# Optimization experiments

Measured on AMD Instinct MI355X. Metric: run time of the kernel, lower is better.

The kernel has to match this reference:

```python
import jax, jax.numpy as jnp
import numpy as np

B, S, I, H, O = 64, 512, 256, 1024, 256


def setup_inputs() -> dict:
    key = jax.random.key(0)
    ks = jax.random.split(key, 12)
    s_in = 1.0 / np.sqrt(H)  # torch RNN init scale
    inp = {
        "x": jax.random.normal(ks[0], (B, S, I), dtype=jnp.float32),
        "W_ih_0": jax.random.uniform(ks[1], (H, I), jnp.float32, -s_in, s_in),
        "W_hh_0": jax.random.uniform(ks[2], (H, H), jnp.float32, -s_in, s_in),
        "b_ih_0": jax.random.uniform(ks[3], (H,), jnp.float32, -s_in, s_in),
        "b_hh_0": jax.random.uniform(ks[4], (H,), jnp.float32, -s_in, s_in),
        "W_ih_1": jax.random.uniform(ks[5], (H, H), jnp.float32, -s_in, s_in),
        "W_hh_1": jax.random.uniform(ks[6], (H, H), jnp.float32, -s_in, s_in),
        "b_ih_1": jax.random.uniform(ks[7], (H,), jnp.float32, -s_in, s_in),
        "b_hh_1": jax.random.uniform(ks[8], (H,), jnp.float32, -s_in, s_in),
        "fc_w": jax.random.uniform(ks[9], (O, H), jnp.float32, -s_in, s_in),
        "fc_b": jax.random.uniform(ks[10], (O,), jnp.float32, -s_in, s_in),
    }
    return inp


def _rnn_layer(inp, W_ih, W_hh, b_ih, b_hh):
    # Pre-compute input projection for all timesteps (one big GEMM),
    # then scan the sequential recurrence: h_t = tanh(Wx_t + U h_{t-1} + b)
    pre = jnp.einsum('bsi,hi->bsh', inp, W_ih) + (b_ih + b_hh)  # [B,S,H]
    h0 = jnp.zeros((inp.shape[0], W_hh.shape[0]), dtype=inp.dtype)

    def step(h, p_t):
        h = jnp.tanh(p_t + h @ W_hh.T)
        return h, h

    _, hs = jax.lax.scan(step, h0, jnp.swapaxes(pre, 0, 1))  # [S,B,H]
    return jnp.swapaxes(hs, 0, 1)  # [B,S,H]


def reference(x, W_ih_0, W_hh_0, b_ih_0, b_hh_0,
              W_ih_1, W_hh_1, b_ih_1, b_hh_1, fc_w, fc_b):
    h = _rnn_layer(x, W_ih_0, W_hh_0, b_ih_0, b_hh_0)
    h = _rnn_layer(h, W_ih_1, W_hh_1, b_ih_1, b_hh_1)
    return h @ fc_w.T + fc_b  # [B,S,O]
```

## Files before the change

### kernel.cpp

```cpp
#include <hip/hip_runtime.h>
#include <hip/hip_bf16.h>


typedef __attribute__((ext_vector_type(4))) float f32x4;
typedef __attribute__((ext_vector_type(8))) short bf16x8;
typedef __attribute__((ext_vector_type(4))) int   i32x4;
typedef __attribute__((ext_vector_type(4))) short s16x4;

#define B_  64
#define S_  512
#define I_  256
#define H_  1024
#define O_  256
#define M_  (B_ * S_)
#define SH_ (S_ * H_)

static __device__ __forceinline__ unsigned short f2bf(float f) {
  union { float f; unsigned u; } v; v.f = f;
  unsigned r = v.u + 0x7fffu + ((v.u >> 16) & 1u);
  return (unsigned short)(r >> 16);
}
static __device__ __forceinline__ float bf2f(unsigned short b) {
  union { unsigned u; float f; } v; v.u = ((unsigned)b) << 16;
  return v.f;
}
static __device__ __forceinline__ float tanh_fast(float x) {
  float e = __expf(2.f * x);
  return 1.f - 2.f / (e + 1.f);
}
static __device__ __forceinline__ bf16x8 as_bf16x8(i32x4 v) {
  union { i32x4 i; bf16x8 b; } u; u.i = v; return u.b;
}

__global__ void cvt_bf16(const float* __restrict__ src,
                         unsigned short* __restrict__ dst, int n4) {
  int i = blockIdx.x * blockDim.x + threadIdx.x;
  if (i < n4) {
    f32x4 v = ((const f32x4*)src)[i];
    s16x4 o;
    o[0] = (short)f2bf(v[0]); o[1] = (short)f2bf(v[1]);
    o[2] = (short)f2bf(v[2]); o[3] = (short)f2bf(v[3]);
    ((s16x4*)dst)[i] = o;
  }
}

template <bool BF16OUT>
__global__ __launch_bounds__(256)
void gemm_bf16(const unsigned short* __restrict__ A,
               const unsigned short* __restrict__ W,
               const float* __restrict__ b1, const float* __restrict__ b2,
               void* __restrict__ Cv, int Mx, int Nx, int Kx) {
  __shared__ __align__(16) unsigned short As[128 * 40];
  __shared__ __align__(16) unsigned short Bs[128 * 40];
  const int tid  = threadIdx.x;
  const int m0   = blockIdx.y * 128;
  const int n0   = blockIdx.x * 128;
  const int w    = tid >> 6, lane = tid & 63;
  const int quad = lane >> 4, l15 = lane & 15;
  const int wm = (w & 1) * 64, wn = (w >> 1) * 64;

  f32x4 acc[4][4] = {};

  for (int k0 = 0; k0 < Kx; k0 += 32) {
#pragma unroll
    for (int i = 0; i < 2; ++i) {
      int c = tid + i * 256;
      int row = c >> 2, kc = c & 3;
      *(i32x4*)&As[row * 40 + kc * 8] =
          *(const i32x4*)&A[(size_t)(m0 + row) * Kx + k0 + kc * 8];
      *(i32x4*)&Bs[row * 40 + kc * 8] =
          *(const i32x4*)&W[(size_t)(n0 + row) * Kx + k0 + kc * 8];
    }
    __syncthreads();
    bf16x8 af[4], bg[4];
#pragma unroll
    for (int im = 0; im < 4; ++im)
      af[im] = *(const bf16x8*)&As[(wm + im * 16 + l15) * 40 + quad * 8];
#pragma unroll
    for (int in = 0; in < 4; ++in)
      bg[in] = *(const bf16x8*)&Bs[(wn + in * 16 + l15) * 40 + quad * 8];
#pragma unroll
    for (int im = 0; im < 4; ++im)
#pragma unroll
      for (int in = 0; in < 4; ++in)
        acc[im][in] = __builtin_amdgcn_mfma_f32_16x16x32_bf16(
            af[im], bg[in], acc[im][in], 0, 0, 0);
    __syncthreads();
  }

#pragma unroll
  for (int in = 0; in < 4; ++in) {
    int n = n0 + wn + in * 16 + l15;
    float bv = b1 ? b1[n] : 0.f;
    if (b2) bv += b2[n];
#pragma unroll
    for (int im = 0; im < 4; ++im) {
      int mb = m0 + wm + im * 16 + quad * 4;
#pragma unroll
      for (int r = 0; r < 4; ++r) {
        float val = acc[im][in][r] + bv;
        size_t o = (size_t)(mb + r) * Nx + n;
        if (BF16OUT) ((unsigned short*)Cv)[o] = f2bf(val);
        else         ((float*)Cv)[o] = val;
      }
    }
  }
}

__global__ __launch_bounds__(256, 1)
void rnn_fused(const unsigned short* __restrict__ Whh0,
               const unsigned short* __restrict__ Wih1,
               const unsigned short* __restrict__ Whh1,
               const unsigned short* __restrict__ pre0,
               const float* __restrict__ b_ih_1,
               const float* __restrict__ b_hh_1,
               unsigned short* __restrict__ h0seq,
               unsigned short* __restrict__ h1seq,
               unsigned int* __restrict__ flags)
{
  const int bx   = blockIdx.x;
  const int tid  = threadIdx.x;
  const int w    = tid >> 6;
  const int lane = tid & 63;
  const int quad = lane >> 4, l15 = lane & 15;

  __shared__ __align__(16) float q[4][4][16][20];

  if (bx < 64) {
    const int g  = bx >> 4;
    const int n0 = (bx & 15) * 64;
    unsigned int* const f0 = flags + g * S_;

    i32x4 Wf[4][8];
    {
      const unsigned short* wp = Whh0 + (size_t)(n0 + l15) * H_ + w * 256 + quad * 8;
#pragma unroll
      for (int i = 0; i < 4; ++i)
#pragma unroll
        for (int kk = 0; kk < 8; ++kk)
          Wf[i][kk] = *(const i32x4*)(wp + (size_t)i * 16 * H_ + kk * 32);
    }
#pragma unroll
    for (int i = 0; i < 4; ++i)
#pragma unroll
      for (int kk = 0; kk < 8; ++kk)
        asm volatile("" : "+v"(Wf[i][kk]));

    for (int t = 0; t < S_; ++t) {
      float pv[4];
      {
        const unsigned short* pp = pre0 + (size_t)(g * 16 + quad * 4) * SH_ +
                                   (size_t)t * H_ + n0 + w * 16 + l15;
#pragma unroll
        for (int r = 0; r < 4; ++r) pv[r] = bf2f(pp[(size_t)r * SH_]);
      }

      f32x4 acc[4] = {};
      if (t > 0) {
        if (tid == 0) {
          while (__hip_atomic_load(&f0[t - 1], __ATOMIC_RELAXED,
                                   __HIP_MEMORY_SCOPE_AGENT) < 16u) {}
          __builtin_amdgcn_fence(__ATOMIC_ACQUIRE, "agent");
        }
        __syncthreads();
        const unsigned short* hp = h0seq + (size_t)(g * 16 + l15) * SH_ +
                                   (size_t)(t - 1) * H_ + w * 256 + quad * 8;
        bf16x8 Af[8];
#pragma unroll
        for (int kk = 0; kk < 8; ++kk) Af[kk] = *(const bf16x8*)(hp + kk * 32);
#pragma unroll
        for (int kk = 0; kk < 8; ++kk)
#pragma unroll
          for (int i = 0; i < 4; ++i)
            acc[i] = __builtin_amdgcn_mfma_f32_16x16x32_bf16(
                Af[kk], as_bf16x8(Wf[i][kk]), acc[i], 0, 0, 0);
      }

#pragma unroll
      for (int i = 0; i < 4; ++i) *(f32x4*)&q[w][i][l15][quad * 4] = acc[i];
      __syncthreads();
      f32x4 s = {};
#pragma unroll
      for (int wp2 = 0; wp2 < 4; ++wp2) {
        f32x4 v = *(const f32x4*)&q[wp2][w][l15][quad * 4];
#pragma unroll
        for (int r = 0; r < 4; ++r) s[r] += v[r];
      }

#pragma unroll
      for (int r = 0; r < 4; ++r) {
        unsigned short hb = f2bf(tanh_fast(pv[r] + s[r]));
        size_t o = (size_t)(g * 16 + quad * 4 + r) * SH_ + (size_t)t * H_ +
                   n0 + w * 16 + l15;
        __hip_atomic_store(&h0seq[o], hb, __ATOMIC_RELAXED,
                           __HIP_MEMORY_SCOPE_AGENT);
      }
      __syncthreads();
      if (tid == 0)
        __hip_atomic_fetch_add(&f0[t], 1u, __ATOMIC_RELAXED,
                               __HIP_MEMORY_SCOPE_AGENT);
    }
  } else {
    const int id = bx - 64;
    const int g  = id >> 5;
    const int n0 = (id & 31) * 32;
    unsigned int* const f0 = flags + g * S_;
    unsigned int* const f1 = flags + 4 * S_ + g * S_;

    i32x4 Wi[2][8], Wr[2][8];
    {
      const unsigned short* wpi = Wih1 + (size_t)(n0 + l15) * H_ + w * 256 + quad * 8;
      const unsigned short* wpr = Whh1 + (size_t)(n0 + l15) * H_ + w * 256 + quad * 8;
#pragma unroll
      for (int i = 0; i < 2; ++i)
#pragma unroll
        for (int kk = 0; kk < 8; ++kk) {
          Wi[i][kk] = *(const i32x4*)(wpi + (size_t)i * 16 * H_ + kk * 32);
          Wr[i][kk] = *(const i32x4*)(wpr + (size_t)i * 16 * H_ + kk * 32);
        }
    }
#pragma unroll
    for (int i = 0; i < 2; ++i)
#pragma unroll
      for (int kk = 0; kk < 8; ++kk) {
        asm volatile("" : "+v"(Wi[i][kk]));
        asm volatile("" : "+v"(Wr[i][kk]));
      }

    float bias = 0.f;
    if (w < 2) {
      int n = n0 + w * 16 + l15;
      bias = b_ih_1[n] + b_hh_1[n];
    }

    for (int t = 0; t < S_; ++t) {
      f32x4 acc[2] = {};

      if (tid == 0) {
        while (__hip_atomic_load(&f0[t], __ATOMIC_RELAXED,
                                 __HIP_MEMORY_SCOPE_AGENT) < 16u) {}
        __builtin_amdgcn_fence(__ATOMIC_ACQUIRE, "agent");
      }
      __syncthreads();
      {
        const unsigned short* hp = h0seq + (size_t)(g * 16 + l15) * SH_ +
                                   (size_t)t * H_ + w * 256 + quad * 8;
        bf16x8 Af[8];
#pragma unroll
        for (int kk = 0; kk < 8; ++kk) Af[kk] = *(const bf16x8*)(hp + kk * 32);
#pragma unroll
        for (int kk = 0; kk < 8; ++kk)
#pragma unroll
          for (int i = 0; i < 2; ++i)
            acc[i] = __builtin_amdgcn_mfma_f32_16x16x32_bf16(
                Af[kk], as_bf16x8(Wi[i][kk]), acc[i], 0, 0, 0);
      }

      if (t > 0) {
        if (tid == 0) {
          while (__hip_atomic_load(&f1[t - 1], __ATOMIC_RELAXED,
                                   __HIP_MEMORY_SCOPE_AGENT) < 32u) {}
          __builtin_amdgcn_fence(__ATOMIC_ACQUIRE, "agent");
        }
        __syncthreads();
        const unsigned short* hp = h1seq + (size_t)(g * 16 + l15) * SH_ +
                                   (size_t)(t - 1) * H_ + w * 256 + quad * 8;
        bf16x8 Af[8];
#pragma unroll
        for (int kk = 0; kk < 8; ++kk) Af[kk] = *(const bf16x8*)(hp + kk * 32);
#pragma unroll
        for (int kk = 0; kk < 8; ++kk)
#pragma unroll
          for (int i = 0; i < 2; ++i)
            acc[i] = __builtin_amdgcn_mfma_f32_16x16x32_bf16(
                Af[kk], as_bf16x8(Wr[i][kk]), acc[i], 0, 0, 0);
      }

#pragma unroll
      for (int i = 0; i < 2; ++i) *(f32x4*)&q[w][i][l15][quad * 4] = acc[i];
      __syncthreads();
      if (w < 2) {
        f32x4 s = {};
#pragma unroll
        for (int wp2 = 0; wp2 < 4; ++wp2) {
          f32x4 v = *(const f32x4*)&q[wp2][w][l15][quad * 4];
#pragma unroll
          for (int r = 0; r < 4; ++r) s[r] += v[r];
        }
#pragma unroll
        for (int r = 0; r < 4; ++r) {
          unsigned short hb = f2bf(tanh_fast(bias + s[r]));
          size_t o = (size_t)(g * 16 + quad * 4 + r) * SH_ + (size_t)t * H_ +
                     n0 + w * 16 + l15;
          __hip_atomic_store(&h1seq[o], hb, __ATOMIC_RELAXED,
                             __HIP_MEMORY_SCOPE_AGENT);
        }
      }
      __syncthreads();
      if (tid == 0)
        __hip_atomic_fetch_add(&f1[t], 1u, __ATOMIC_RELAXED,
                               __HIP_MEMORY_SCOPE_AGENT);
    }
  }
}

extern "C" void kernel_launch(void* const* d_in, const int* in_sizes, int n_in,
                              void* d_out, int out_size, void* d_ws, size_t ws_size,
                              hipStream_t stream) {
  const float* x      = (const float*)d_in[0];
  const float* W_ih_0 = (const float*)d_in[1];
  const float* W_hh_0 = (const float*)d_in[2];
  const float* b_ih_0 = (const float*)d_in[3];
  const float* b_hh_0 = (const float*)d_in[4];
  const float* W_ih_1 = (const float*)d_in[5];
  const float* W_hh_1 = (const float*)d_in[6];
  const float* b_ih_1 = (const float*)d_in[7];
  const float* b_hh_1 = (const float*)d_in[8];
  const float* fc_w   = (const float*)d_in[9];
  const float* fc_b   = (const float*)d_in[10];
  float* out = (float*)d_out;

  char* ws = (char*)d_ws;
  size_t off = 0;
  auto alloc = [&](size_t bytes) { char* p = ws + off; off += (bytes + 255) & ~(size_t)255; return p; };
  unsigned short* xb    = (unsigned short*)alloc((size_t)M_ * I_ * 2);
  unsigned short* wih0b = (unsigned short*)alloc((size_t)H_ * I_ * 2);
  unsigned short* whh0b = (unsigned short*)alloc((size_t)H_ * H_ * 2);
  unsigned short* wih1b = (unsigned short*)alloc((size_t)H_ * H_ * 2);
  unsigned short* whh1b = (unsigned short*)alloc((size_t)H_ * H_ * 2);
  unsigned short* fcwb  = (unsigned short*)alloc((size_t)O_ * H_ * 2);
  unsigned int*   flags = (unsigned int*)alloc(2 * 4 * S_ * 4);
  unsigned short* pre0b = (unsigned short*)alloc((size_t)M_ * H_ * 2);
  unsigned short* h0seq = (unsigned short*)alloc((size_t)M_ * H_ * 2);
  unsigned short* h1seq = (unsigned short*)alloc((size_t)M_ * H_ * 2);

  hipMemsetAsync(flags, 0, 2 * 4 * S_ * 4, stream);

  auto cvt = [&](const float* s, unsigned short* d, int n) {
    int n4 = n / 4;
    cvt_bf16<<<(n4 + 255) / 256, 256, 0, stream>>>(s, d, n4);
  };
  cvt(x,      xb,    M_ * I_);
  cvt(W_ih_0, wih0b, H_ * I_);
  cvt(W_hh_0, whh0b, H_ * H_);
  cvt(W_ih_1, wih1b, H_ * H_);
  cvt(W_hh_1, whh1b, H_ * H_);
  cvt(fc_w,   fcwb,  O_ * H_);

  gemm_bf16<true><<<dim3(H_ / 128, M_ / 128), 256, 0, stream>>>(
      xb, wih0b, b_ih_0, b_hh_0, pre0b, M_, H_, I_);

  rnn_fused<<<192, 256, 0, stream>>>(whh0b, wih1b, whh1b, pre0b,
                                     b_ih_1, b_hh_1, h0seq, h1seq, flags);

  gemm_bf16<false><<<dim3(O_ / 128, M_ / 128), 256, 0, stream>>>(
      h1seq, fcwb, fc_b, nullptr, out, M_, O_, H_);
}
```

Baseline: 2.815 ms.

## Replace block-wide atomic counters with per-wave flag arrays polled by whole waves

Each wave now publishes its own per-timestep flag with a release store, instead of one thread per block doing a relaxed fetch_add on a shared counter. Consumers poll all 64 producer flags at once, one lane per flag, and use a wave-wide __all vote. This removes contention on a single counter and drops the tid==0 spin plus __syncthreads on the critical path of every recurrent step. In exchange the flag buffer grows 64x and every wave issues its own polling loads, which adds memory traffic.

```diff
diff --git a/kernel.cpp b/kernel.cpp
--- a/kernel.cpp
+++ b/kernel.cpp
@@ -30,6 +30,16 @@
 }
 static __device__ __forceinline__ bf16x8 as_bf16x8(i32x4 v) {
   union { i32x4 i; bf16x8 b; } u; u.i = v; return u.b;
+}
+
+static __device__ __forceinline__ void wait64(const unsigned* __restrict__ p,
+                                              int lane) {
+  unsigned v;
+  do {
+    v = __hip_atomic_load(p + lane, __ATOMIC_RELAXED,
+                          __HIP_MEMORY_SCOPE_AGENT);
+  } while (!__all(v != 0u));
+  __builtin_amdgcn_fence(__ATOMIC_ACQUIRE, "agent");
 }
 
 __global__ void cvt_bf16(const float* __restrict__ src,
@@ -107,7 +117,8 @@
   }
 }
 
-__global__ __launch_bounds__(256, 1)
+__global__ __launch_bounds__(256)
+__attribute__((amdgpu_waves_per_eu(1, 1)))
 void rnn_fused(const unsigned short* __restrict__ Whh0,
                const unsigned short* __restrict__ Wih1,
                const unsigned short* __restrict__ Whh1,
@@ -126,10 +137,14 @@
 
   __shared__ __align__(16) float q[4][4][16][20];
 
+  unsigned int* const F0 = flags;
+  unsigned int* const F1 = flags + 4 * S_ * 64;
+
   if (bx < 64) {
     const int g  = bx >> 4;
-    const int n0 = (bx & 15) * 64;
-    unsigned int* const f0 = flags + g * S_;
+    const int j  = bx & 15;
+    const int n0 = j * 64;
+    unsigned int* const f0 = F0 + (size_t)g * S_ * 64;
 
     i32x4 Wf[4][8];
     {
@@ -157,12 +172,7 @@
 
       f32x4 acc[4] = {};
       if (t > 0) {
-        if (tid == 0) {
-          while (__hip_atomic_load(&f0[t - 1], __ATOMIC_RELAXED,
-                                   __HIP_MEMORY_SCOPE_AGENT) < 16u) {}
-          __builtin_amdgcn_fence(__ATOMIC_ACQUIRE, "agent");
-        }
-        __syncthreads();
+        wait64(f0 + (size_t)(t - 1) * 64, lane);
         const unsigned short* hp = h0seq + (size_t)(g * 16 + l15) * SH_ +
                                    (size_t)(t - 1) * H_ + w * 256 + quad * 8;
         bf16x8 Af[8];
@@ -195,17 +205,18 @@
         __hip_atomic_store(&h0seq[o], hb, __ATOMIC_RELAXED,
                            __HIP_MEMORY_SCOPE_AGENT);
       }
+      if (lane == 0)
+        __hip_atomic_store(&f0[(size_t)t * 64 + j * 4 + w], 1u,
+                           __ATOMIC_RELEASE, __HIP_MEMORY_SCOPE_AGENT);
       __syncthreads();
-      if (tid == 0)
-        __hip_atomic_fetch_add(&f0[t], 1u, __ATOMIC_RELAXED,
-                               __HIP_MEMORY_SCOPE_AGENT);
     }
   } else {
     const int id = bx - 64;
     const int g  = id >> 5;
-    const int n0 = (id & 31) * 32;
-    unsigned int* const f0 = flags + g * S_;
-    unsigned int* const f1 = flags + 4 * S_ + g * S_;
+    const int j  = id & 31;
+    const int n0 = j * 32;
+    unsigned int* const f0 = F0 + (size_t)g * S_ * 64;
+    unsigned int* const f1 = F1 + (size_t)g * S_ * 64;
 
     i32x4 Wi[2][8], Wr[2][8];
     {
@@ -236,12 +247,7 @@
     for (int t = 0; t < S_; ++t) {
       f32x4 acc[2] = {};
 
-      if (tid == 0) {
-        while (__hip_atomic_load(&f0[t], __ATOMIC_RELAXED,
-                                 __HIP_MEMORY_SCOPE_AGENT) < 16u) {}
-        __builtin_amdgcn_fence(__ATOMIC_ACQUIRE, "agent");
-      }
-      __syncthreads();
+      wait64(f0 + (size_t)t * 64, lane);
       {
         const unsigned short* hp = h0seq + (size_t)(g * 16 + l15) * SH_ +
                                    (size_t)t * H_ + w * 256 + quad * 8;
@@ -257,12 +263,7 @@
       }
 
       if (t > 0) {
-        if (tid == 0) {
-          while (__hip_atomic_load(&f1[t - 1], __ATOMIC_RELAXED,
-                                   __HIP_MEMORY_SCOPE_AGENT) < 32u) {}
-          __builtin_amdgcn_fence(__ATOMIC_ACQUIRE, "agent");
-        }
-        __syncthreads();
+        wait64(f1 + (size_t)(t - 1) * 64, lane);
         const unsigned short* hp = h1seq + (size_t)(g * 16 + l15) * SH_ +
                                    (size_t)(t - 1) * H_ + w * 256 + quad * 8;
         bf16x8 Af[8];
@@ -295,11 +296,11 @@
           __hip_atomic_store(&h1seq[o], hb, __ATOMIC_RELAXED,
                              __HIP_MEMORY_SCOPE_AGENT);
         }
+        if (lane == 0)
+          __hip_atomic_store(&f1[(size_t)t * 64 + j * 2 + w], 1u,
+                             __ATOMIC_RELEASE, __HIP_MEMORY_SCOPE_AGENT);
       }
       __syncthreads();
-      if (tid == 0)
-        __hip_atomic_fetch_add(&f1[t], 1u, __ATOMIC_RELAXED,
-                               __HIP_MEMORY_SCOPE_AGENT);
     }
   }
 }
@@ -329,12 +330,13 @@
   unsigned short* wih1b = (unsigned short*)alloc((size_t)H_ * H_ * 2);
   unsigned short* whh1b = (unsigned short*)alloc((size_t)H_ * H_ * 2);
   unsigned short* fcwb  = (unsigned short*)alloc((size_t)O_ * H_ * 2);
-  unsigned int*   flags = (unsigned int*)alloc(2 * 4 * S_ * 4);
+  const size_t flagBytes = (size_t)2 * 4 * S_ * 64 * 4;
+  unsigned int*   flags = (unsigned int*)alloc(flagBytes);
   unsigned short* pre0b = (unsigned short*)alloc((size_t)M_ * H_ * 2);
   unsigned short* h0seq = (unsigned short*)alloc((size_t)M_ * H_ * 2);
   unsigned short* h1seq = (unsigned short*)alloc((size_t)M_ * H_ * 2);
 
-  hipMemsetAsync(flags, 0, 2 * 4 * S_ * 4, stream);
+  hipMemsetAsync(flags, 0, flagBytes, stream);
 
   auto cvt = [&](const float* s, unsigned short* d, int n) {
     int n4 = n / 4;
```

Measured after the change: 8.920 ms. 217% more time.
